# Performance work log

Hardware: AMD Instinct MI355X
Metric: run time of the kernel (lower is better)

## Reference

```python
import jax, jax.numpy as jnp
import numpy as np

B, S, D, H, DK = 2, 2048, 1024, 16, 64
NEG = -1000000000.0


def setup_inputs() -> dict:
    key = jax.random.key(0)
    ks = jax.random.split(key, 7)
    scale = 1.0 / np.sqrt(D)
    return {
        "pos_encode_toks": jax.random.normal(ks[0], (B, S, D), dtype=jnp.float32),
        "Wq": jax.random.uniform(ks[1], (D, D), minval=-scale, maxval=scale, dtype=jnp.float32),
        "bq": jax.random.uniform(ks[2], (D,), minval=-scale, maxval=scale, dtype=jnp.float32),
        "Wk": jax.random.uniform(ks[3], (D, D), minval=-scale, maxval=scale, dtype=jnp.float32),
        "bk": jax.random.uniform(ks[4], (D,), minval=-scale, maxval=scale, dtype=jnp.float32),
        "W0": jax.random.uniform(ks[5], (D, D), minval=-scale, maxval=scale, dtype=jnp.float32),
        "b0": jax.random.uniform(ks[6], (D,), minval=-scale, maxval=scale, dtype=jnp.float32),
    }


def reference(pos_encode_toks, Wq, bq, Wk, bk, W0, b0):
    x = pos_encode_toks
    b, s, d = x.shape
    # NOTE: the original module computes V with Wq (a bug in the source) -- replicated here.
    q = (x @ Wq + bq).reshape(b, s, H, DK).transpose(0, 2, 1, 3)  # [B,H,S,DK]
    k = (x @ Wk + bk).reshape(b, s, H, DK).transpose(0, 2, 1, 3)
    v = q  # V = Wq(x), same projection as Q
    scores = jnp.einsum("bhqd,bhkd->bhqk", q, k) / np.sqrt(DK)
    causal = jnp.tril(jnp.ones((s, s), dtype=bool))
    scores = jnp.where(causal, scores, NEG)
    att_pat = jax.nn.softmax(scores, axis=-1)
    att = jnp.einsum("bhqk,bhkd->bhqd", att_pat, v)
    att = att.transpose(0, 2, 1, 3).reshape(b, s, d)
    return att @ W0 + b0
```

## Files before the change

kernel.cpp:

```cpp
#include <hip/hip_runtime.h>
#include <hip/hip_bf16.h>
#include <cstdint>
#include <cstddef>


#define AS1 __attribute__((address_space(1)))
#define AS3 __attribute__((address_space(3)))

typedef unsigned short u16;
typedef __attribute__((ext_vector_type(8))) short bf16x8;
typedef __attribute__((ext_vector_type(4))) float f32x4;

__device__ __forceinline__ u16 f2bf(float f) {
  uint32_t u = __builtin_bit_cast(uint32_t, f);
  u += 0x7fffu + ((u >> 16) & 1u);
  return (u16)(u >> 16);
}
__device__ __forceinline__ uint32_t pk2bf(float a, float b) {
  return (uint32_t)f2bf(a) | ((uint32_t)f2bf(b) << 16);
}

__device__ __forceinline__ void gload16(const void* g, void* l) {
  __builtin_amdgcn_global_load_lds((const AS1 uint32_t*)(uintptr_t)g,
                                   (AS3 uint32_t*)(uintptr_t)l, 16, 0, 0);
}

#define SCALE2 0.18033688011112042f

__global__ __launch_bounds__(256) void prep_kernel(
    const float* __restrict__ x, u16* __restrict__ xb,
    const float* __restrict__ Wq, const float* __restrict__ Wk,
    const float* __restrict__ W0, u16* __restrict__ wqT,
    u16* __restrict__ wkT, u16* __restrict__ w0T) {
  __shared__ u16 T[64][65];
  const int bid = blockIdx.x;
  if (bid < 1024) {
    const float4* x4 = (const float4*)x;
    ushort4* o4 = (ushort4*)xb;
    for (int i = bid * 256 + threadIdx.x; i < 1048576; i += 262144) {
      float4 v = x4[i];
      ushort4 o;
      o.x = f2bf(v.x); o.y = f2bf(v.y); o.z = f2bf(v.z); o.w = f2bf(v.w);
      o4[i] = o;
    }
    return;
  }
  const int t = bid - 1024;
  const int z = t >> 8, y = (t >> 4) & 15, xt = t & 15;
  const float* src; u16* dst;
  if (z == 0)      { src = Wq; dst = wqT; }
  else if (z == 1) { src = Wk; dst = wkT; }
  else             { src = W0; dst = w0T; }
  const int k0 = y * 64, n0 = xt * 64;
  const int c = threadIdx.x & 63, r0 = threadIdx.x >> 6;
#pragma unroll
  for (int i = 0; i < 16; ++i) {
    int r = i * 4 + r0;
    T[r][c] = f2bf(src[(size_t)(k0 + r) * 1024 + n0 + c]);
  }
  __syncthreads();
#pragma unroll
  for (int i = 0; i < 16; ++i) {
    int r = i * 4 + r0;
    dst[(size_t)(n0 + r) * 1024 + k0 + c] = T[c][r];
  }
}

template <int EPI, int NTILES>
__global__ __launch_bounds__(512, 4) void gemm_kernel(
    const u16* __restrict__ A, const u16* __restrict__ BT,
    const float* __restrict__ bias0, const float* __restrict__ bias1,
    u16* __restrict__ Oq, u16* __restrict__ Ok, u16* __restrict__ OqT,
    float* __restrict__ Of) {
  __shared__ __align__(16) u16 As[128][64];
  __shared__ __align__(16) u16 Bs[128][64];
  const int tid = threadIdx.x, wid = tid >> 6, lane = tid & 63;
  const int l15 = lane & 15, lg = lane >> 4;
  constexpr int NH = NTILES / 2;
  const int bid = blockIdx.x;
  const int c = bid & 7, l = bid >> 3;
  const int m0 = ((c >> 1) * 8 + l / NH) * 128;
  const int n0 = ((c & 1) * NH + l % NH) * 128;
  const int wrow = (wid >> 2) * 64, wcol = (wid & 3) * 32;
  const int srow = lane >> 3;
  const int gz = ((lane & 7) ^ srow) * 8;

  f32x4 acc[4][2] = {};

  for (int k0 = 0; k0 < 1024; k0 += 64) {
#pragma unroll
    for (int i = 0; i < 2; ++i) {
      int ch = wid * 2 + i;
      gload16(&A[(size_t)(m0 + ch * 8 + srow) * 1024 + k0 + gz], &As[ch * 8][0]);
      gload16(&BT[(size_t)(n0 + ch * 8 + srow) * 1024 + k0 + gz], &Bs[ch * 8][0]);
    }
    __syncthreads();
#pragma unroll
    for (int kf = 0; kf < 2; ++kf) {
      const int cg = ((kf * 4 + lg) ^ (lane & 7)) * 8;
      bf16x8 af[4], bfr[2];
#pragma unroll
      for (int m = 0; m < 4; ++m)
        af[m] = *(const bf16x8*)&As[wrow + m * 16 + l15][cg];
#pragma unroll
      for (int n = 0; n < 2; ++n)
        bfr[n] = *(const bf16x8*)&Bs[wcol + n * 16 + l15][cg];
#pragma unroll
      for (int m = 0; m < 4; ++m)
#pragma unroll
        for (int n = 0; n < 2; ++n)
          acc[m][n] = __builtin_amdgcn_mfma_f32_16x16x32_bf16(af[m], bfr[n], acc[m][n], 0, 0, 0);
    }
    __syncthreads();
  }

  const bool isq = (n0 < 1024);
  float bv[2];
#pragma unroll
  for (int n = 0; n < 2; ++n) {
    const int gn = n0 + wcol + n * 16 + l15;
    if constexpr (EPI == 0)
      bv[n] = isq ? bias0[gn] : bias1[gn - 1024];
    else
      bv[n] = bias0[gn];
  }
#pragma unroll
  for (int m = 0; m < 4; ++m) {
#pragma unroll
    for (int r = 0; r < 4; ++r) {
      const int gm = m0 + wrow + m * 16 + lg * 4 + r;
#pragma unroll
      for (int n = 0; n < 2; ++n) {
        const int gn = n0 + wcol + n * 16 + l15;
        float v = acc[m][n][r] + bv[n];
        if constexpr (EPI == 2) {
          Of[(size_t)gm * 1024 + gn] = v;
        } else {
          const int gg = gn & 1023;
          const int b = gm >> 11, s = gm & 2047;
          const int h = gg >> 6, dk = gg & 63;
          const size_t bh = (size_t)(b * 16 + h);
          if (isq) {
            const u16 qb = f2bf(v);
            Oq[(bh * 2048 + s) * 64 + dk] = qb;
            OqT[(bh * 64 + dk) * 2048 + s] = qb;
          } else {
            Ok[(bh * 2048 + s) * 64 + dk] = f2bf(v * SCALE2);
          }
        }
      }
    }
  }
}

__global__ __launch_bounds__(256, 4) void attn_kernel(const u16* __restrict__ Q,
                                                      const u16* __restrict__ K,
                                                      const u16* __restrict__ QT,
                                                      u16* __restrict__ ATT) {
  __shared__ __align__(16) u16 Ks[2][64][64];
  __shared__ __align__(16) u16 Vs[2][64][64];
  __shared__ __align__(16) u16 Ps[4][16][64];
  const int tid = threadIdx.x, wid = tid >> 6, lane = tid & 63;
  const int l15 = lane & 15, lg = lane >> 4;
  const int bid = blockIdx.x;
  const int bh = bid & 31;
  const int qt = 31 - (bid >> 5);
  const size_t base = (size_t)bh * 2048 * 64;
  const int bb = bh >> 4, hh = bh & 15;
  const int srow = lane >> 3;
  const int gz = ((lane & 7) ^ srow) * 8;

  const int q0 = qt * 64;
  const int wrow = q0 + wid * 16;

  bf16x8 qf[2];
#pragma unroll
  for (int kf = 0; kf < 2; ++kf)
    qf[kf] = *(const bf16x8*)&Q[base + (size_t)(wrow + l15) * 64 + kf * 32 + lg * 8];

  f32x4 o[4] = {};
  float mx = -3e38f, sm = 0.f;

#pragma unroll
  for (int i = 0; i < 2; ++i) {
    int ch = wid * 2 + i;
    gload16(&K[base + (size_t)(ch * 8 + srow) * 64 + gz], &Ks[0][ch * 8][0]);
    gload16(&QT[base + (size_t)(ch * 8 + srow) * 2048 + gz], &Vs[0][ch * 8][0]);
  }
  __syncthreads();

  for (int t = 0; t <= qt; ++t) {
    const int cur = t & 1;
    if (t < qt) {
      const int kv1 = (t + 1) * 64;
#pragma unroll
      for (int i = 0; i < 2; ++i) {
        int ch = wid * 2 + i;
        gload16(&K[base + (size_t)(kv1 + ch * 8 + srow) * 64 + gz], &Ks[cur ^ 1][ch * 8][0]);
        gload16(&QT[base + (size_t)(ch * 8 + srow) * 2048 + kv1 + gz], &Vs[cur ^ 1][ch * 8][0]);
      }
    }

    f32x4 sc[4] = {};
#pragma unroll
    for (int kf = 0; kf < 2; ++kf) {
      const int cg = ((kf * 4 + lg) ^ (lane & 7)) * 8;
      bf16x8 kb[4];
#pragma unroll
      for (int n = 0; n < 4; ++n)
        kb[n] = *(const bf16x8*)&Ks[cur][n * 16 + l15][cg];
      __builtin_amdgcn_s_setprio(1);
#pragma unroll
      for (int n = 0; n < 4; ++n)
        sc[n] = __builtin_amdgcn_mfma_f32_16x16x32_bf16(kb[n], qf[kf], sc[n], 0, 0, 0);
      __builtin_amdgcn_s_setprio(0);
    }

    if (t == qt) {
      const int qq = wid * 16 + l15;
#pragma unroll
      for (int n = 0; n < 4; ++n)
#pragma unroll
        for (int r = 0; r < 4; ++r)
          if (n * 16 + lg * 4 + r > qq) sc[n][r] = -1e30f;
    }

    float ma = fmaxf(fmaxf(sc[0][0], sc[0][1]), fmaxf(sc[0][2], sc[0][3]));
    float mb = fmaxf(fmaxf(sc[1][0], sc[1][1]), fmaxf(sc[1][2], sc[1][3]));
    float mc = fmaxf(fmaxf(sc[2][0], sc[2][1]), fmaxf(sc[2][2], sc[2][3]));
    float md = fmaxf(fmaxf(sc[3][0], sc[3][1]), fmaxf(sc[3][2], sc[3][3]));
    float rmax = fmaxf(fmaxf(ma, mb), fmaxf(mc, md));
    rmax = fmaxf(rmax, __shfl_xor(rmax, 16));
    rmax = fmaxf(rmax, __shfl_xor(rmax, 32));

    if (__any(rmax > mx + 8.0f)) {
      const float mnew = fmaxf(mx, rmax);
      const float alpha = exp2f(mx - mnew);
      mx = mnew;
      sm *= alpha;
#pragma unroll
      for (int m = 0; m < 4; ++m) o[m] *= alpha;
    }

    float psum = 0.f;
    uint32_t w[4][2];
#pragma unroll
    for (int n = 0; n < 4; ++n) {
      const float p0 = exp2f(sc[n][0] - mx), p1 = exp2f(sc[n][1] - mx);
      const float p2 = exp2f(sc[n][2] - mx), p3 = exp2f(sc[n][3] - mx);
      psum += (p0 + p1) + (p2 + p3);
      w[n][0] = pk2bf(p0, p1);
      w[n][1] = pk2bf(p2, p3);
    }
    sm += psum;

#pragma unroll
    for (int n = 0; n < 4; ++n) {
      const int col = (((2 * n + (lg >> 1)) ^ (l15 & 7)) << 3) + ((lg & 1) << 2);
      uint2 wv; wv.x = w[n][0]; wv.y = w[n][1];
      *(uint2*)&Ps[wid][l15][col] = wv;
    }
    asm volatile("s_waitcnt lgkmcnt(0)" ::: "memory");

#pragma unroll
    for (int kf = 0; kf < 2; ++kf) {
      const int cg = ((kf * 4 + lg) ^ (lane & 7)) * 8;
      bf16x8 pb = *(const bf16x8*)&Ps[wid][l15][cg];
      bf16x8 vb[4];
#pragma unroll
      for (int m = 0; m < 4; ++m)
        vb[m] = *(const bf16x8*)&Vs[cur][m * 16 + l15][cg];
      __builtin_amdgcn_s_setprio(1);
#pragma unroll
      for (int m = 0; m < 4; ++m)
        o[m] = __builtin_amdgcn_mfma_f32_16x16x32_bf16(vb[m], pb, o[m], 0, 0, 0);
      __builtin_amdgcn_s_setprio(0);
    }
    __syncthreads();
  }

  sm += __shfl_xor(sm, 16);
  sm += __shfl_xor(sm, 32);
  const float inv = 1.0f / sm;
  const int s = wrow + l15;
#pragma unroll
  for (int m = 0; m < 4; ++m) {
    uint2 wv;
    wv.x = pk2bf(o[m][0] * inv, o[m][1] * inv);
    wv.y = pk2bf(o[m][2] * inv, o[m][3] * inv);
    *(uint2*)&ATT[((size_t)(bb * 2048 + s)) * 1024 + hh * 64 + m * 16 + lg * 4] = wv;
  }
}

extern "C" void kernel_launch(void* const* d_in, const int* in_sizes, int n_in,
                              void* d_out, int out_size, void* d_ws, size_t ws_size,
                              hipStream_t stream) {
  const float* x  = (const float*)d_in[0];
  const float* Wq = (const float*)d_in[1];
  const float* bq = (const float*)d_in[2];
  const float* Wk = (const float*)d_in[3];
  const float* bk = (const float*)d_in[4];
  const float* W0 = (const float*)d_in[5];
  const float* b0 = (const float*)d_in[6];
  float* out = (float*)d_out;

  char* ws = (char*)d_ws;
  u16* xb  = (u16*)(ws + 0);
  u16* wqT = (u16*)(ws + 8388608);
  u16* wkT = (u16*)(ws + 10485760);
  u16* w0T = (u16*)(ws + 12582912);
  u16* q   = (u16*)(ws + 14680064);
  u16* k   = (u16*)(ws + 23068672);
  u16* qT  = (u16*)(ws + 31457280);
  u16* att = (u16*)(ws + 39845888);

  prep_kernel<<<dim3(1792), dim3(256), 0, stream>>>(x, xb, Wq, Wk, W0, wqT, wkT, w0T);
  gemm_kernel<0, 16><<<dim3(512), dim3(512), 0, stream>>>(xb, wqT, bq, bk, q, k, qT, nullptr);
  attn_kernel<<<dim3(1024), dim3(256), 0, stream>>>(q, k, qT, att);
  gemm_kernel<2, 8><<<dim3(256), dim3(512), 0, stream>>>(att, w0T, b0, nullptr, nullptr, nullptr, nullptr, out);
}
```

Before: 181.4 us.

## Move Q transpose to separate kernel, pad P tile, precompute attention load pointers

The strided transposed-Q store is removed from the QKV GEMM epilogue and done instead by a dedicated LDS-tiled transpose kernel, so the GEMM writes only coalesced outputs. The attention kernel pads the P scratch buffer rows to 72 elements to reduce LDS bank conflicts, and it precomputes the K/V global and LDS pointers so the double-buffered prefetch needs less address arithmetic. The trade-off is an extra kernel launch plus a re-read of Q from memory.

```diff
diff --git a/kernel.cpp b/kernel.cpp
--- a/kernel.cpp
+++ b/kernel.cpp
@@ -1,5 +1,4 @@
 #include <hip/hip_runtime.h>
-#include <hip/hip_bf16.h>
 #include <cstdint>
 #include <cstddef>
 
@@ -66,12 +65,32 @@
   }
 }
 
+__global__ __launch_bounds__(256) void transpose_q_kernel(const u16* __restrict__ q,
+                                                          u16* __restrict__ qT) {
+  const int bh = blockIdx.y;
+  const int s0 = blockIdx.x * 64;
+  const u16* src = q + (size_t)bh * 2048 * 64;
+  u16* dst = qT + (size_t)bh * 64 * 2048;
+  __shared__ u16 T[64][65];
+  const int c = threadIdx.x & 63, r0 = threadIdx.x >> 6;
+#pragma unroll
+  for (int i = 0; i < 16; ++i) {
+    int r = i * 4 + r0;
+    T[r][c] = src[(size_t)(s0 + r) * 64 + c];
+  }
+  __syncthreads();
+#pragma unroll
+  for (int i = 0; i < 16; ++i) {
+    int r = i * 4 + r0;
+    dst[(size_t)r * 2048 + s0 + c] = T[c][r];
+  }
+}
+
 template <int EPI, int NTILES>
 __global__ __launch_bounds__(512, 4) void gemm_kernel(
     const u16* __restrict__ A, const u16* __restrict__ BT,
     const float* __restrict__ bias0, const float* __restrict__ bias1,
-    u16* __restrict__ Oq, u16* __restrict__ Ok, u16* __restrict__ OqT,
-    float* __restrict__ Of) {
+    u16* __restrict__ Oq, u16* __restrict__ Ok, float* __restrict__ Of) {
   __shared__ __align__(16) u16 As[128][64];
   __shared__ __align__(16) u16 Bs[128][64];
   const int tid = threadIdx.x, wid = tid >> 6, lane = tid & 63;
@@ -141,9 +160,7 @@
           const int h = gg >> 6, dk = gg & 63;
           const size_t bh = (size_t)(b * 16 + h);
           if (isq) {
-            const u16 qb = f2bf(v);
-            Oq[(bh * 2048 + s) * 64 + dk] = qb;
-            OqT[(bh * 64 + dk) * 2048 + s] = qb;
+            Oq[(bh * 2048 + s) * 64 + dk] = f2bf(v);
           } else {
             Ok[(bh * 2048 + s) * 64 + dk] = f2bf(v * SCALE2);
           }
@@ -159,7 +176,7 @@
                                                       u16* __restrict__ ATT) {
   __shared__ __align__(16) u16 Ks[2][64][64];
   __shared__ __align__(16) u16 Vs[2][64][64];
-  __shared__ __align__(16) u16 Ps[4][16][64];
+  __shared__ __align__(16) u16 Ps[4][16][72];
   const int tid = threadIdx.x, wid = tid >> 6, lane = tid & 63;
   const int l15 = lane & 15, lg = lane >> 4;
   const int bid = blockIdx.x;
@@ -173,6 +190,16 @@
   const int q0 = qt * 64;
   const int wrow = q0 + wid * 16;
 
+  const u16* kA  = K  + base + (size_t)(wid * 16 + srow) * 64 + gz;
+  const u16* kB  = kA + 8 * 64;
+  const u16* vA  = QT + base + (size_t)(wid * 16 + srow) * 2048 + gz;
+  const u16* vB  = vA + 8 * 2048;
+  u16* ldsKA = &Ks[0][wid * 16][0];
+  u16* ldsKB = &Ks[0][wid * 16 + 8][0];
+  u16* ldsVA = &Vs[0][wid * 16][0];
+  u16* ldsVB = &Vs[0][wid * 16 + 8][0];
+  const int bufo = 64 * 64;
+
   bf16x8 qf[2];
 #pragma unroll
   for (int kf = 0; kf < 2; ++kf)
@@ -181,24 +208,18 @@
   f32x4 o[4] = {};
   float mx = -3e38f, sm = 0.f;
 
-#pragma unroll
-  for (int i = 0; i < 2; ++i) {
-    int ch = wid * 2 + i;
-    gload16(&K[base + (size_t)(ch * 8 + srow) * 64 + gz], &Ks[0][ch * 8][0]);
-    gload16(&QT[base + (size_t)(ch * 8 + srow) * 2048 + gz], &Vs[0][ch * 8][0]);
-  }
+  gload16(kA, ldsKA); gload16(kB, ldsKB);
+  gload16(vA, ldsVA); gload16(vB, ldsVB);
   __syncthreads();
 
   for (int t = 0; t <= qt; ++t) {
     const int cur = t & 1;
     if (t < qt) {
-      const int kv1 = (t + 1) * 64;
-#pragma unroll
-      for (int i = 0; i < 2; ++i) {
-        int ch = wid * 2 + i;
-        gload16(&K[base + (size_t)(kv1 + ch * 8 + srow) * 64 + gz], &Ks[cur ^ 1][ch * 8][0]);
-        gload16(&QT[base + (size_t)(ch * 8 + srow) * 2048 + kv1 + gz], &Vs[cur ^ 1][ch * 8][0]);
-      }
+      const int nxt = (cur ^ 1) * bufo;
+      gload16(kA + (t + 1) * 4096, ldsKA + nxt);
+      gload16(kB + (t + 1) * 4096, ldsKB + nxt);
+      gload16(vA + (t + 1) * 64,   ldsVA + nxt);
+      gload16(vB + (t + 1) * 64,   ldsVB + nxt);
     }
 
     f32x4 sc[4] = {};
@@ -315,7 +336,8 @@
   u16* att = (u16*)(ws + 39845888);
 
   prep_kernel<<<dim3(1792), dim3(256), 0, stream>>>(x, xb, Wq, Wk, W0, wqT, wkT, w0T);
-  gemm_kernel<0, 16><<<dim3(512), dim3(512), 0, stream>>>(xb, wqT, bq, bk, q, k, qT, nullptr);
+  gemm_kernel<0, 16><<<dim3(512), dim3(512), 0, stream>>>(xb, wqT, bq, bk, q, k, nullptr);
+  transpose_q_kernel<<<dim3(32, 32), dim3(256), 0, stream>>>(q, qT);
   attn_kernel<<<dim3(1024), dim3(256), 0, stream>>>(q, k, qT, att);
-  gemm_kernel<2, 8><<<dim3(256), dim3(512), 0, stream>>>(att, w0T, b0, nullptr, nullptr, nullptr, nullptr, out);
-}
+  gemm_kernel<2, 8><<<dim3(256), dim3(512), 0, stream>>>(att, w0T, b0, nullptr, nullptr, nullptr, out);
+}
```

Result: no change. 182.5 us (+0.6%).
